# Kernel tuning notes

Hardware: AMD Instinct MI355X
Metric: run time of the kernel (lower is better)

Reference implementation:

```python
import jax, jax.numpy as jnp
import numpy as np
from jax import lax

# ---- static config (matches init_kwargs) ----
STRIDE = 16
BASE_SIZE = 16
SCALES = np.array([2., 4., 8., 16., 32.])
RATIOS = np.array([0.5, 1., 2.])
CLIP = 4.14
NMS_THRESH = 0.7
PRE_NMS = 6000
POST_NMS = 300
MIN_SIZE = 16.0


def _whctrs(a):
    w = a[2] - a[0] + 1.0
    h = a[3] - a[1] + 1.0
    return w, h, a[0] + 0.5 * (w - 1.0), a[1] + 0.5 * (h - 1.0)


def _mkanchors(ws, hs, xc, yc):
    return np.stack([xc - 0.5 * (ws - 1.0), yc - 0.5 * (hs - 1.0),
                     xc + 0.5 * (ws - 1.0), yc + 0.5 * (hs - 1.0)], axis=1)


def _base_anchors():
    ba = np.array([1.0, 1.0, BASE_SIZE, BASE_SIZE]) - 1.0
    w, h, xc, yc = _whctrs(ba)
    size = w * h
    ws = np.round(np.sqrt(size / RATIOS))
    hs = np.round(ws * RATIOS)
    ra = _mkanchors(ws, hs, xc, yc)
    out = []
    for i in range(ra.shape[0]):
        w, h, xc, yc = _whctrs(ra[i])
        out.append(_mkanchors(w * SCALES, h * SCALES, xc, yc))
    return np.concatenate(out, axis=0)  # (A,4), A = len(ratios)*len(scales)


def _grid_anchors(Hf, Wf):
    ba = _base_anchors()                       # (A,4)
    sx, sy = np.meshgrid(np.arange(Wf) * STRIDE, np.arange(Hf) * STRIDE)
    shifts = np.stack([sx, sy, sx, sy], axis=-1)          # (Hf,Wf,4)
    anch = shifts[:, :, None, :] + ba[None, None, :, :]    # (Hf,Wf,A,4)
    return jnp.asarray(anch.reshape(1, -1, 4), dtype=jnp.float32)


def _decode_clip(anchors, deltas, img_h, img_w):
    # NormalizedBoxCenterDecoder (stds=1) + clip to image
    aw = anchors[..., 2] - anchors[..., 0]
    ah = anchors[..., 3] - anchors[..., 1]
    ax = anchors[..., 0] + 0.5 * aw
    ay = anchors[..., 1] + 0.5 * ah
    dx, dy, dw, dh = deltas[..., 0], deltas[..., 1], deltas[..., 2], deltas[..., 3]
    ox = dx * aw + ax
    oy = dy * ah + ay
    ow = jnp.exp(jnp.minimum(dw, CLIP)) * aw * 0.5
    oh = jnp.exp(jnp.minimum(dh, CLIP)) * ah * 0.5
    x1 = jnp.clip(ox - ow, 0.0, img_w - 1.0)
    y1 = jnp.clip(oy - oh, 0.0, img_h - 1.0)
    x2 = jnp.clip(ox + ow, 0.0, img_w - 1.0)
    y2 = jnp.clip(oy + oh, 0.0, img_h - 1.0)
    return jnp.stack([x1, y1, x2, y2], axis=-1)


def _nms_single(scores, boxes):
    # scores (N,), boxes (N,4). Greedy NMS, force_suppress, sorted by score desc.
    order = jnp.argsort(-scores)[:PRE_NMS]
    s = scores[order]
    b = boxes[order]
    x1, y1, x2, y2 = b[:, 0], b[:, 1], b[:, 2], b[:, 3]
    area = (x2 - x1) * (y2 - y1)
    iw = jnp.maximum(jnp.minimum(x2[:, None], x2[None, :]) - jnp.maximum(x1[:, None], x1[None, :]), 0.0)
    ih = jnp.maximum(jnp.minimum(y2[:, None], y2[None, :]) - jnp.maximum(y1[:, None], y1[None, :]), 0.0)
    inter = iw * ih
    iou = inter / (area[:, None] + area[None, :] - inter + 1e-12)  # (PRE,PRE)

    supp0 = s < 0.0  # invalid entries (score set to -1 by min_size filter)

    def body(supp, i):
        keep = jnp.logical_not(supp[i])
        new = jnp.where(keep, jnp.logical_or(supp, iou[i] > NMS_THRESH), supp)
        new = new.at[i].set(supp[i])  # never self-suppress
        return new, None

    supp, _ = lax.scan(body, supp0, jnp.arange(PRE_NMS))
    kept = jnp.logical_not(supp)
    perm = jnp.argsort(jnp.where(kept, 0, 1), stable=True)  # kept boxes first, order preserved
    out_s = jnp.where(kept[perm], s[perm], -1.0)
    out_b = jnp.where(kept[perm][:, None], b[perm], -1.0)
    return out_s[:POST_NMS, None], out_b[:POST_NMS]


def _forward(img, x, conv_w, conv_b, score_w, score_b, loc_w, loc_b):
    B, _, Hf, Wf = x.shape
    img_h, img_w = float(img.shape[2]), float(img.shape[3])
    anchors = _grid_anchors(Hf, Wf)  # (1, Hf*Wf*A, 4)

    # conv1 3x3 pad 1 + ReLU
    h = lax.conv_general_dilated(x, conv_w, (1, 1), [(1, 1), (1, 1)],
                                 dimension_numbers=('NCHW', 'OIHW', 'NCHW'))
    h = jax.nn.relu(h + conv_b[None, :, None, None])

    A = score_w.shape[0]
    raw_scores = jnp.einsum('bchw,oc->bhwo', h, score_w.reshape(A, -1)) + score_b
    raw_scores = raw_scores.reshape(B, -1, 1)                       # (B,N,1)
    raw_boxes = jnp.einsum('bchw,oc->bhwo', h, loc_w.reshape(4 * A, -1)) + loc_b
    raw_boxes = raw_boxes.reshape(B, -1, 4)                         # (B,N,4)

    rpn_scores = jax.nn.sigmoid(raw_scores)

    roi = _decode_clip(anchors, raw_boxes, img_h, img_w)            # (B,N,4)
    width = roi[..., 2] - roi[..., 0]
    height = roi[..., 3] - roi[..., 1]
    invalid = jnp.logical_or(width < MIN_SIZE, height < MIN_SIZE)   # (B,N)
    score = jnp.where(invalid[..., None], -1.0, rpn_scores)         # (B,N,1)
    roi = jnp.where(invalid[..., None], -1.0, roi)

    out_s, out_b = jax.vmap(_nms_single)(score[..., 0], roi)        # (B,300,1),(B,300,4)
    return jnp.concatenate([out_s, out_b], axis=-1)                 # (B,300,5)


def setup_inputs() -> dict:
    key = jax.random.key(0)
    ks = jax.random.split(key, 8)
    img = jax.random.normal(ks[0], (1, 3, 1024, 1024), jnp.float32)
    x = jax.random.normal(ks[1], (1, 1024, 64, 64), jnp.float32)
    conv_w = jax.random.normal(ks[2], (1024, 1024, 3, 3), jnp.float32) * 0.01
    conv_b = jnp.zeros((1024,), jnp.float32)
    score_w = jax.random.normal(ks[3], (15, 1024, 1, 1), jnp.float32) * 0.01
    score_b = jnp.zeros((15,), jnp.float32)
    loc_w = jax.random.normal(ks[4], (60, 1024, 1, 1), jnp.float32) * 0.002
    loc_b = jnp.zeros((60,), jnp.float32)
    return {"img": img, "x": x, "conv_w": conv_w, "conv_b": conv_b,
            "score_w": score_w, "score_b": score_b, "loc_w": loc_w, "loc_b": loc_b}


def reference(img, x, conv_w, conv_b, score_w, score_b, loc_w, loc_b):
    return _forward(img, x, conv_w, conv_b, score_w, score_b, loc_w, loc_b)
```

## Files before the change

### kernel.cpp

```cpp
#include <hip/hip_runtime.h>

typedef unsigned int uint;
typedef unsigned short ushort;
typedef unsigned long long u64;

typedef __attribute__((ext_vector_type(8))) short short8;
typedef __attribute__((ext_vector_type(4))) float floatx4;

__device__ inline ushort bf16rne(float v) {
  uint b = __float_as_uint(v);
  uint r = (b + 0x7fffu + ((b >> 16) & 1u)) >> 16;
  return (ushort)r;
}

__device__ inline void gl_lds16(const void* g, void* l) {
  __builtin_amdgcn_global_load_lds(
      (const __attribute__((address_space(1))) unsigned int*)g,
      (__attribute__((address_space(3))) unsigned int*)l, 16, 0, 0);
}


__global__ __launch_bounds__(256) void prep_x(const float* __restrict__ x,
                                              ushort* __restrict__ xh,
                                              ushort* __restrict__ xl) {
  __shared__ float tile[8][512];
  int cc = blockIdx.x, sg = blockIdx.y, t = threadIdx.x;
  int ci0 = cc * 32 + sg * 8;
  size_t obase = (size_t)(cc * 4 + sg) * 4356;
  for (int it = 0; it < 4; ++it) {
    int s0 = blockIdx.z * 2048 + it * 512;
#pragma unroll
    for (int e = 0; e < 8; ++e) {
      tile[e][t] = x[(size_t)(ci0 + e) * 4096 + s0 + t];
      tile[e][t + 256] = x[(size_t)(ci0 + e) * 4096 + s0 + 256 + t];
    }
    __syncthreads();
#pragma unroll
    for (int w = 0; w < 2; ++w) {
      int sl = w * 256 + t;
      int s = s0 + sl;
      int y = s >> 6, xx = s & 63;
      short8 sh, slo;
#pragma unroll
      for (int e = 0; e < 8; ++e) {
        float v = tile[e][sl];
        ushort h2 = bf16rne(v);
        float hf = __uint_as_float((uint)h2 << 16);
        sh[e] = (short)h2;
        slo[e] = (short)bf16rne(v - hf);
      }
      size_t o = (obase + (size_t)(y + 1) * 66 + (xx + 1)) * 8;
      *(short8*)(xh + o) = sh;
      *(short8*)(xl + o) = slo;
    }
    __syncthreads();
  }
}

__global__ __launch_bounds__(256) void prep_w(const float* __restrict__ w,
                                              ushort* __restrict__ wh,
                                              ushort* __restrict__ wl) {
  int cc = blockIdx.x, sg = blockIdx.y, t = threadIdx.x;
  int e = t & 7, col = t >> 3;
  int ci = cc * 32 + sg * 8 + e;
  for (int chunk = 0; chunk < 8; ++chunk) {
    int co = blockIdx.z * 256 + chunk * 32 + col;
    const float* src = w + ((size_t)co * 1024 + ci) * 9;
    float v[9];
#pragma unroll
    for (int o = 0; o < 9; ++o) v[o] = src[o];
#pragma unroll
    for (int off = 0; off < 9; ++off) {
      ushort h2 = bf16rne(v[off]);
      float hf = __uint_as_float((uint)h2 << 16);
      ushort l2 = bf16rne(v[off] - hf);
      size_t oi = ((size_t)(off * 32 + cc) * 4 + sg) * 8192 + (size_t)co * 8 + e;
      wh[oi] = h2;
      wl[oi] = l2;
    }
  }
}

__global__ __launch_bounds__(256) void prep_head(
    const float* __restrict__ score_w, const float* __restrict__ loc_w,
    const float* __restrict__ score_b, const float* __restrict__ loc_b,
    ushort* __restrict__ wh, ushort* __restrict__ wl, float* __restrict__ bh) {
  int idx = blockIdx.x * 256 + threadIdx.x;
  int o = idx >> 10, ci = idx & 1023;
  float v = 0.f;
  if (o < 15) v = score_w[o * 1024 + ci];
  else if (o < 75) v = loc_w[(o - 15) * 1024 + ci];
  ushort h2 = bf16rne(v);
  float hf = __uint_as_float((uint)h2 << 16);
  int cc = ci >> 5, sg = (ci >> 3) & 3, e = ci & 7;
  size_t oi = ((size_t)(cc * 4 + sg) * 128 + o) * 8 + e;
  wh[oi] = h2;
  wl[oi] = bf16rne(v - hf);
  if (idx < 128) bh[idx] = (idx < 15) ? score_b[idx] : ((idx < 75) ? loc_b[idx - 15] : 0.f);
}

template <int IM2COL, int BM, int BN>
__global__ __launch_bounds__(256, 1) void gemm_bf16x3(
    const ushort* __restrict__ Ahi, const ushort* __restrict__ Alo,
    const ushort* __restrict__ Bhi, const ushort* __restrict__ Blo,
    const float* __restrict__ bias, int nChunks, float* __restrict__ outRaw,
    ushort* __restrict__ outHi, ushort* __restrict__ outLo) {
  constexpr int ASEC = BM * 32;
  constexpr int BUFU = 2 * ASEC;
  constexpr int WM = (BM >= 128) ? 2 : 1;
  constexpr int WN = 4 / WM;
  constexpr int MI = (BM / WM) / 16;
  constexpr int NJ = (BN / WN) / 16;
  __shared__ ushort sm[2 * BUFU];
  const int t = threadIdx.x;
  const int m0 = blockIdx.x * BM;
  const int n0 = blockIdx.y * BN;

  const int lane = t & 63, wv = t >> 6;
  const int wm = (wv % WM) * (BM / WM);
  const int wn = (wv / WM) * (BN / WN);
  const int rA = wm + (lane & 15);
  const int segA = (lane >> 4) * (BM * 16);

  auto stage = [&](int c, int bufIdx) {
    ushort* secAh = sm + bufIdx * BUFU;
    ushort* secAl = secAh + ASEC;
    int cc = 0, oy = 0, ox = 0;
    if (IM2COL) {
      int off = c >> 5;
      cc = c & 31;
      oy = off / 3;
      ox = off - 3 * oy;
    }
    for (int L = t; L < BM * 4; L += 256) {
      int row = L % BM, seg = L / BM;
      size_t aoff;
      if (IM2COL) {
        int m = m0 + row, y = m >> 6, xq = m & 63;
        aoff = ((size_t)(cc * 4 + seg) * 4356 + (y + oy) * 66 + (xq + ox)) * 16;
      } else {
        aoff = ((size_t)(c * 4 + seg) * 4096 + (m0 + row)) * 16;
      }
      gl_lds16((const char*)Ahi + aoff, (char*)secAh + L * 16);
      gl_lds16((const char*)Alo + aoff, (char*)secAl + L * 16);
    }
  };

  auto loadB = [&](int c, short8* bh, short8* bl) {
    int sg = lane >> 4;
#pragma unroll
    for (int j = 0; j < NJ; ++j) {
      int co = n0 + wn + (lane & 15) + 16 * j;
      size_t boff;
      if (IM2COL) {
        int off = c >> 5, cc = c & 31;
        boff = (((size_t)(off * 32 + cc) * 4 + sg) * 1024 + co) * 16;
      } else {
        boff = (((size_t)(c * 4 + sg)) * 128 + co) * 16;
      }
      bh[j] = *(const short8*)((const char*)Bhi + boff);
      bl[j] = *(const short8*)((const char*)Blo + boff);
    }
  };

  floatx4 acc[MI][NJ];
#pragma unroll
  for (int i = 0; i < MI; ++i)
#pragma unroll
    for (int j = 0; j < NJ; ++j) acc[i][j] = (floatx4){0.f, 0.f, 0.f, 0.f};

  auto compute = [&](const ushort* sb, const short8* bh2, const short8* bl2) {
    const char* cAh = (const char*)sb;
    const char* cAl = (const char*)(sb + ASEC);
    short8 ah[MI], al[MI];
#pragma unroll
    for (int i = 0; i < MI; ++i) {
      int pa = segA + (rA + 16 * i) * 16;
      ah[i] = *(const short8*)(cAh + pa);
      al[i] = *(const short8*)(cAl + pa);
    }
#pragma unroll
    for (int i = 0; i < MI; ++i)
#pragma unroll
      for (int j = 0; j < NJ; ++j) {
        acc[i][j] = __builtin_amdgcn_mfma_f32_16x16x32_bf16(ah[i], bh2[j], acc[i][j], 0, 0, 0);
        acc[i][j] = __builtin_amdgcn_mfma_f32_16x16x32_bf16(ah[i], bl2[j], acc[i][j], 0, 0, 0);
        acc[i][j] = __builtin_amdgcn_mfma_f32_16x16x32_bf16(al[i], bh2[j], acc[i][j], 0, 0, 0);
      }
  };

  short8 b0h[NJ], b0l[NJ], b1h[NJ], b1l[NJ];
  stage(0, 0);
  loadB(0, b0h, b0l);
  for (int kc = 0; kc < nChunks; kc += 2) {
    __syncthreads();
    if (kc + 1 < nChunks) { stage(kc + 1, 1); loadB(kc + 1, b1h, b1l); }
    compute(sm, b0h, b0l);
    __syncthreads();
    if (kc + 2 < nChunks) { stage(kc + 2, 0); loadB(kc + 2, b0h, b0l); }
    compute(sm + BUFU, b1h, b1l);
  }

#pragma unroll
  for (int i = 0; i < MI; ++i)
#pragma unroll
    for (int j = 0; j < NJ; ++j) {
      int nn = n0 + wn + 16 * j + (lane & 15);
      float bv = bias[nn];
#pragma unroll
      for (int r = 0; r < 4; ++r) {
        int mm = m0 + wm + 16 * i + (lane >> 4) * 4 + r;
        float v = acc[i][j][r] + bv;
        if (IM2COL) {
          v = fmaxf(v, 0.f);
          ushort h2 = bf16rne(v);
          float hf = __uint_as_float((uint)h2 << 16);
          ushort l2 = bf16rne(v - hf);
          int cc = nn >> 5, sg = (nn >> 3) & 3, e = nn & 7;
          size_t ho = ((size_t)(cc * 4 + sg) * 4096 + mm) * 8 + e;
          outHi[ho] = h2;
          outLo[ho] = l2;
        } else {
          outRaw[(size_t)mm * 128 + nn] = v;
        }
      }
    }
}

__global__ __launch_bounds__(256) void decode_k(const float* __restrict__ raw,
                                                float* __restrict__ scores,
                                                float4* __restrict__ boxes,
                                                uint* __restrict__ key32,
                                                uint* __restrict__ hist) {
  int i = blockIdx.x * 256 + threadIdx.x;
  int m = i / 15, a = i - m * 15;
  int y = m >> 6, x = m & 63;
  const float* rp = raw + (size_t)m * 128;
  float logit = rp[a];
  float dx = rp[15 + 4 * a], dy = rp[16 + 4 * a];
  float dw = rp[17 + 4 * a], dh = rp[18 + 4 * a];
  int rr = a / 5, ss = a - rr * 5;
  float sc5 = (float)(2 << ss);
  float W = ((rr == 0) ? 23.f : (rr == 1) ? 16.f : 11.f) * sc5;
  float H = ((rr == 0) ? 12.f : (rr == 1) ? 16.f : 22.f) * sc5;
  float aw = W - 1.f, ah = H - 1.f;
  float ax = x * 16.f + 7.5f, ay = y * 16.f + 7.5f;
  float ox = dx * aw + ax, oyc = dy * ah + ay;
  float ow = expf(fminf(dw, 4.14f)) * aw * 0.5f;
  float oh = expf(fminf(dh, 4.14f)) * ah * 0.5f;
  float x1 = fminf(fmaxf(ox - ow, 0.f), 1023.f);
  float y1 = fminf(fmaxf(oyc - oh, 0.f), 1023.f);
  float x2 = fminf(fmaxf(ox + ow, 0.f), 1023.f);
  float y2 = fminf(fmaxf(oyc + oh, 0.f), 1023.f);
  bool inval = ((x2 - x1) < 16.f) || ((y2 - y1) < 16.f);
  float sc = inval ? -1.f : (1.f / (1.f + expf(-logit)));
  scores[i] = sc;
  boxes[i] = inval ? make_float4(-1.f, -1.f, -1.f, -1.f) : make_float4(x1, y1, x2, y2);
  uint kb = __float_as_uint(sc);
  uint key = (kb & 0x80000000u) ? ~kb : (kb | 0x80000000u);
  key32[i] = key;
  atomicAdd(&hist[key >> 16], 1u);
}

__global__ __launch_bounds__(256) void seg_sum(const uint* __restrict__ hist,
                                               uint* __restrict__ segsum) {
  __shared__ uint red[256];
  int b = blockIdx.x, t = threadIdx.x;
  red[t] = hist[b * 256 + t];
  __syncthreads();
  for (int d = 128; d > 0; d >>= 1) {
    if (t < d) red[t] += red[t + d];
    __syncthreads();
  }
  if (t == 0) segsum[b] = red[0];
}

__global__ __launch_bounds__(256) void find_t16(const uint* __restrict__ hist,
                                                const uint* __restrict__ segsum,
                                                uint* __restrict__ selT) {
  __shared__ uint ps[256];
  __shared__ int segS;
  int t = threadIdx.x;
  ps[t] = segsum[t];
  __syncthreads();
  for (int d = 1; d < 256; d <<= 1) {
    uint v = ps[t] + ((t + d < 256) ? ps[t + d] : 0u);
    __syncthreads();
    ps[t] = v;
    __syncthreads();
  }
  if (ps[t] >= 6000u && (t == 255 || ps[t + 1] < 6000u)) segS = t;
  __syncthreads();
  int sg = segS;
  uint base = (sg == 255) ? 0u : ps[sg + 1];
  uint h2 = hist[sg * 256 + t];
  __syncthreads();
  ps[t] = h2;
  __syncthreads();
  for (int d = 1; d < 256; d <<= 1) {
    uint v = ps[t] + ((t + d < 256) ? ps[t + d] : 0u);
    __syncthreads();
    ps[t] = v;
    __syncthreads();
  }
  if (base + ps[t] >= 6000u && (t == 255 || base + ps[t + 1] < 6000u))
    *selT = (uint)(sg * 256 + t);
}

__global__ __launch_bounds__(256) void gather_k(const uint* __restrict__ key32,
                                                const uint* __restrict__ selT,
                                                uint* __restrict__ cnt,
                                                u64* __restrict__ cand) {
  int i = blockIdx.x * 256 + threadIdx.x;
  uint T = *selT;
  uint k = key32[i];
  if ((k >> 16) >= T) {
    uint pos = atomicAdd(cnt, 1u);
    if (pos < 8192) cand[pos] = ((u64)k << 32) | (u64)(~(uint)i);
  }
}

__global__ __launch_bounds__(1024) void sort_gather(
    const u64* __restrict__ cand, const uint* __restrict__ cnt,
    const float* __restrict__ scores, const float4* __restrict__ boxes,
    float* __restrict__ sortedS, float4* __restrict__ sortedB) {
  extern __shared__ u64 sk[];
  int t = threadIdx.x;
  int C = (int)*cnt;
  if (C > 8192) C = 8192;
  for (int j = t; j < 8192; j += 1024) sk[j] = (j < C) ? cand[j] : 0ull;
  __syncthreads();
  for (int k = 2; k <= 8192; k <<= 1) {
    for (int j2 = k >> 1; j2 > 0; j2 >>= 1) {
      for (int p = t; p < 4096; p += 1024) {
        int i = ((p & ~(j2 - 1)) << 1) | (p & (j2 - 1));
        int ix = i | j2;
        u64 a = sk[i], b = sk[ix];
        bool ddir = (i & k) != 0;
        if ((a < b) != ddir) { sk[i] = b; sk[ix] = a; }
      }
      __syncthreads();
    }
  }
  for (int j = t; j < 6016; j += 1024) {
    if (j < 6000) {
      u64 key = sk[j];
      uint idx = ~(uint)(key & 0xffffffffu);
      sortedS[j] = scores[idx];
      sortedB[j] = boxes[idx];
    } else {
      sortedS[j] = -1.f;
      sortedB[j] = make_float4(0.f, 0.f, 0.f, 0.f);
    }
  }
}

__global__ __launch_bounds__(64) void iou_mask(const float4* __restrict__ boxes,
                                               u64* __restrict__ mask) {
  __shared__ float cx1[64], cy1[64], cx2[64], cy2[64], car[64];
  int bi = blockIdx.x, bj = blockIdx.y, t = threadIdx.x;
  float4 cb = boxes[bj * 64 + t];
  cx1[t] = cb.x; cy1[t] = cb.y; cx2[t] = cb.z; cy2[t] = cb.w;
  car[t] = (cb.z - cb.x) * (cb.w - cb.y);
  __syncthreads();
  int r = bi * 64 + t;
  float4 rb = boxes[r];
  float ra = (rb.z - rb.x) * (rb.w - rb.y);
  u64 wd = 0;
#pragma unroll 8
  for (int j = 0; j < 64; ++j) {
    float iw = fmaxf(fminf(rb.z, cx2[j]) - fmaxf(rb.x, cx1[j]), 0.f);
    float ih = fmaxf(fminf(rb.w, cy2[j]) - fmaxf(rb.y, cy1[j]), 0.f);
    float inter = iw * ih;
    float iou = inter / (ra + car[j] - inter + 1e-12f);
    if (iou > 0.7f && r != bj * 64 + j) wd |= (1ull << j);
  }
  mask[(size_t)r * 128 + bj] = wd;
}

__global__ __launch_bounds__(64) void nms_scan(const u64* __restrict__ mask,
                                               const float* __restrict__ sortedS,
                                               const float4* __restrict__ sortedB,
                                               float* __restrict__ out) {
  __shared__ int klist[300];
  int lane = threadIdx.x;
  u64 Sx = 0, Sy = 0;
  for (int w2 = 0; w2 < 94; ++w2) {
    bool neg = sortedS[w2 * 64 + lane] < 0.f;
    u64 m2 = __ballot(neg);
    if ((w2 >> 1) == lane) { if (w2 & 1) Sy = m2; else Sx = m2; }
  }
  int count = 0;
  for (int w2 = 0; w2 < 94; ++w2) {
    u64 cur = __shfl((w2 & 1) ? Sy : Sx, w2 >> 1);
    u64 rem = ~cur;
    if (w2 == 93) rem &= (1ull << 48) - 1;
    if (!rem) continue;
    int bA = __builtin_ctzll(rem);
    ulonglong2 vA = ((const ulonglong2*)(mask + (size_t)(w2 * 64 + bA) * 128))[lane];
    int bB;
    ulonglong2 vB;
    for (;;) {
      {
        u64 remS = (bA == 63) ? 0ull : (rem & (~0ull << (bA + 1)));
        bB = remS ? __builtin_ctzll(remS) : -1;
        if (bB >= 0)
          vB = ((const ulonglong2*)(mask + (size_t)(w2 * 64 + bB) * 128))[lane];
        if (lane == 0) klist[count] = w2 * 64 + bA;
        count++;
        if (count == 300) goto done;
        Sx |= vA.x;
        Sy |= vA.y;
        u64 cur2 = __shfl((w2 & 1) ? Sy : Sx, w2 >> 1);
        rem = remS & ~cur2;
        if (!rem) break;
        int bn = __builtin_ctzll(rem);
        if (bn != bB) {
          bB = bn;
          vB = ((const ulonglong2*)(mask + (size_t)(w2 * 64 + bB) * 128))[lane];
        }
      }
      {
        u64 remS = (bB == 63) ? 0ull : (rem & (~0ull << (bB + 1)));
        bA = remS ? __builtin_ctzll(remS) : -1;
        if (bA >= 0)
          vA = ((const ulonglong2*)(mask + (size_t)(w2 * 64 + bA) * 128))[lane];
        if (lane == 0) klist[count] = w2 * 64 + bB;
        count++;
        if (count == 300) goto done;
        Sx |= vB.x;
        Sy |= vB.y;
        u64 cur2 = __shfl((w2 & 1) ? Sy : Sx, w2 >> 1);
        rem = remS & ~cur2;
        if (!rem) break;
        int bn = __builtin_ctzll(rem);
        if (bn != bA) {
          bA = bn;
          vA = ((const ulonglong2*)(mask + (size_t)(w2 * 64 + bA) * 128))[lane];
        }
      }
    }
  }
done:
  __syncthreads();
  for (int j = lane; j < 300; j += 64) {
    float s;
    float4 bb;
    if (j < count) {
      int i = klist[j];
      s = sortedS[i];
      bb = sortedB[i];
    } else {
      s = -1.f;
      bb = make_float4(-1.f, -1.f, -1.f, -1.f);
    }
    out[j * 5 + 0] = s;
    out[j * 5 + 1] = bb.x;
    out[j * 5 + 2] = bb.y;
    out[j * 5 + 3] = bb.z;
    out[j * 5 + 4] = bb.w;
  }
}

constexpr size_t O_XH = 0;
constexpr size_t O_XL = 8921088;
constexpr size_t O_WTH = 17842176;
constexpr size_t O_WTL = 36716544;
constexpr size_t O_HH = 55590912;
constexpr size_t O_HL = 63979520;
constexpr size_t O_WHH = 72368128;
constexpr size_t O_WHL = 72630272;
constexpr size_t O_BHD = 72892416;
constexpr size_t O_SC = 72892928;
constexpr size_t O_BX = 73138688;
constexpr size_t O_KEY = 74121728;
constexpr size_t O_HIST = 74367488;
constexpr size_t O_CNT = 74629632;
constexpr size_t O_CAND = 74629888;
constexpr size_t O_SELT = 74695424;
constexpr size_t O_SS = 74695680;
constexpr size_t O_SB = 74719744;
constexpr size_t O_RAW = 0;
constexpr size_t O_MASK = 17842176;
constexpr size_t O_SEG = 24002560;

extern "C" void kernel_launch(void* const* d_in, const int* in_sizes, int n_in,
                              void* d_out, int out_size, void* d_ws,
                              size_t ws_size, hipStream_t stream) {
  (void)in_sizes; (void)n_in; (void)out_size; (void)ws_size;
  const float* x = (const float*)d_in[1];
  const float* conv_w = (const float*)d_in[2];
  const float* conv_b = (const float*)d_in[3];
  const float* score_w = (const float*)d_in[4];
  const float* score_b = (const float*)d_in[5];
  const float* loc_w = (const float*)d_in[6];
  const float* loc_b = (const float*)d_in[7];
  float* out = (float*)d_out;
  char* ws = (char*)d_ws;

  ushort* xh = (ushort*)(ws + O_XH);
  ushort* xl = (ushort*)(ws + O_XL);
  ushort* wTh = (ushort*)(ws + O_WTH);
  ushort* wTl = (ushort*)(ws + O_WTL);
  ushort* hh = (ushort*)(ws + O_HH);
  ushort* hl = (ushort*)(ws + O_HL);
  ushort* wHh = (ushort*)(ws + O_WHH);
  ushort* wHl = (ushort*)(ws + O_WHL);
  float* biasH = (float*)(ws + O_BHD);
  float* raw = (float*)(ws + O_RAW);
  float* scores = (float*)(ws + O_SC);
  float4* boxes = (float4*)(ws + O_BX);
  uint* key32 = (uint*)(ws + O_KEY);
  uint* hist = (uint*)(ws + O_HIST);
  uint* cnt = (uint*)(ws + O_CNT);
  u64* cand = (u64*)(ws + O_CAND);
  uint* selT = (uint*)(ws + O_SELT);
  float* sortedS = (float*)(ws + O_SS);
  float4* sortedB = (float4*)(ws + O_SB);
  u64* mask = (u64*)(ws + O_MASK);
  uint* segsum = (uint*)(ws + O_SEG);

  hipMemsetAsync(ws + O_XH, 0, 2 * 8921088, stream);
  hipMemsetAsync(ws + O_HIST, 0, 262144 + 256, stream);

  prep_x<<<dim3(32, 4, 2), 256, 0, stream>>>(x, xh, xl);
  prep_w<<<dim3(32, 4, 4), 256, 0, stream>>>(conv_w, wTh, wTl);
  prep_head<<<512, 256, 0, stream>>>(score_w, loc_w, score_b, loc_b, wHh, wHl, biasH);

  gemm_bf16x3<1, 128, 64><<<dim3(32, 16), 256, 0, stream>>>(
      xh, xl, wTh, wTl, conv_b, 288, nullptr, hh, hl);
  gemm_bf16x3<0, 32, 128><<<dim3(128, 1), 256, 0, stream>>>(
      hh, hl, wHh, wHl, biasH, 32, raw, nullptr, nullptr);

  decode_k<<<240, 256, 0, stream>>>(raw, scores, boxes, key32, hist);
  seg_sum<<<256, 256, 0, stream>>>(hist, segsum);
  find_t16<<<1, 256, 0, stream>>>(hist, segsum, selT);
  gather_k<<<240, 256, 0, stream>>>(key32, selT, cnt, cand);
  sort_gather<<<1, 1024, 65536, stream>>>(cand, cnt, scores, boxes, sortedS, sortedB);
  iou_mask<<<dim3(94, 94), 64, 0, stream>>>(sortedB, mask);
  nms_scan<<<1, 64, 0, stream>>>(mask, sortedS, sortedB, out);
}
```

Baseline: 715.3 us.

## Split conv GEMM into triple-buffered kernel staging B through LDS

The 3x3 conv GEMM gets its own kernel. Both A and B tiles now stream into LDS through async global-to-LDS loads, with a three-deep ring buffer and explicit vmcnt waits, so there is one barrier per K chunk instead of register-loaded B with double buffering. Launch bounds now allow two blocks per CU. The head GEMM keeps the old path. The aim is to hide global memory latency and raise occupancy, at the cost of more LDS use per block and fragile hand-tuned waitcnt ordering.

```diff
diff --git a/kernel.cpp b/kernel.cpp
--- a/kernel.cpp
+++ b/kernel.cpp
@@ -99,12 +99,132 @@
   if (idx < 128) bh[idx] = (idx < 15) ? score_b[idx] : ((idx < 75) ? loc_b[idx - 15] : 0.f);
 }
 
-template <int IM2COL, int BM, int BN>
-__global__ __launch_bounds__(256, 1) void gemm_bf16x3(
+__global__ __launch_bounds__(256, 2) void gemm_conv(
     const ushort* __restrict__ Ahi, const ushort* __restrict__ Alo,
     const ushort* __restrict__ Bhi, const ushort* __restrict__ Blo,
-    const float* __restrict__ bias, int nChunks, float* __restrict__ outRaw,
-    ushort* __restrict__ outHi, ushort* __restrict__ outLo) {
+    const float* __restrict__ bias, ushort* __restrict__ outHi,
+    ushort* __restrict__ outLo) {
+  constexpr int NC = 288;
+  constexpr int ASEC = 128 * 32;
+  constexpr int BSEC = 64 * 32;
+  constexpr int BUFU = 2 * ASEC + 2 * BSEC;
+  __shared__ ushort sm[3 * BUFU];
+  const int t = threadIdx.x;
+  const int m0 = blockIdx.x * 128;
+  const int n0 = blockIdx.y * 64;
+
+  const int lane = t & 63, wv = t >> 6;
+  const int wm = (wv & 1) * 64, wn = (wv >> 1) * 32;
+  const int rA = wm + (lane & 15);
+  const int rB = wn + (lane & 15);
+  const int segA = (lane >> 4) * 2048;
+  const int segB = (lane >> 4) * 1024;
+
+  auto stage = [&](int c, ushort* buf) {
+    ushort* secAh = buf;
+    ushort* secAl = buf + ASEC;
+    ushort* secBh = buf + 2 * ASEC;
+    ushort* secBl = buf + 2 * ASEC + BSEC;
+    int off = c >> 5, cc = c & 31;
+    int oy = off / 3, ox = off - 3 * oy;
+#pragma unroll
+    for (int q = 0; q < 2; ++q) {
+      int L = t + 256 * q;
+      int row = L & 127, seg = L >> 7;
+      int m = m0 + row, y = m >> 6, xq = m & 63;
+      size_t aoff = ((size_t)(cc * 4 + seg) * 4356 + (y + oy) * 66 + (xq + ox)) * 16;
+      gl_lds16((const char*)Ahi + aoff, (char*)secAh + L * 16);
+      gl_lds16((const char*)Alo + aoff, (char*)secAl + L * 16);
+    }
+    {
+      int L = t;
+      int row = L & 63, seg = L >> 6;
+      size_t boff = (((size_t)(off * 32 + cc) * 4 + seg) * 1024 + (n0 + row)) * 16;
+      gl_lds16((const char*)Bhi + boff, (char*)secBh + L * 16);
+      gl_lds16((const char*)Blo + boff, (char*)secBl + L * 16);
+    }
+  };
+
+  floatx4 acc[4][2];
+#pragma unroll
+  for (int i = 0; i < 4; ++i)
+#pragma unroll
+    for (int j = 0; j < 2; ++j) acc[i][j] = (floatx4){0.f, 0.f, 0.f, 0.f};
+
+  auto compute = [&](const ushort* sb) {
+    const char* cAh = (const char*)sb;
+    const char* cAl = (const char*)(sb + ASEC);
+    const char* cBh = (const char*)(sb + 2 * ASEC);
+    const char* cBl = (const char*)(sb + 2 * ASEC + BSEC);
+    short8 ah[4], al[4], bh2[2], bl2[2];
+#pragma unroll
+    for (int i = 0; i < 4; ++i) {
+      int pa = segA + (rA + 16 * i) * 16;
+      ah[i] = *(const short8*)(cAh + pa);
+      al[i] = *(const short8*)(cAl + pa);
+    }
+#pragma unroll
+    for (int j = 0; j < 2; ++j) {
+      int pb = segB + (rB + 16 * j) * 16;
+      bh2[j] = *(const short8*)(cBh + pb);
+      bl2[j] = *(const short8*)(cBl + pb);
+    }
+#pragma unroll
+    for (int i = 0; i < 4; ++i)
+#pragma unroll
+      for (int j = 0; j < 2; ++j) {
+        acc[i][j] = __builtin_amdgcn_mfma_f32_16x16x32_bf16(ah[i], bh2[j], acc[i][j], 0, 0, 0);
+        acc[i][j] = __builtin_amdgcn_mfma_f32_16x16x32_bf16(ah[i], bl2[j], acc[i][j], 0, 0, 0);
+        acc[i][j] = __builtin_amdgcn_mfma_f32_16x16x32_bf16(al[i], bh2[j], acc[i][j], 0, 0, 0);
+      }
+  };
+
+  stage(0, sm);
+  stage(1, sm + BUFU);
+  int br = 0;
+  int bw = 2;
+  for (int kc = 0; kc < NC; ++kc) {
+    __builtin_amdgcn_sched_barrier(0);
+    if (kc < NC - 1) {
+      asm volatile("s_waitcnt vmcnt(6)" ::: "memory");
+    } else {
+      asm volatile("s_waitcnt vmcnt(0)" ::: "memory");
+    }
+    __builtin_amdgcn_sched_barrier(0);
+    __builtin_amdgcn_s_barrier();
+    __builtin_amdgcn_sched_barrier(0);
+    if (kc + 2 < NC) stage(kc + 2, sm + bw * BUFU);
+    compute(sm + br * BUFU);
+    br = (br == 2) ? 0 : br + 1;
+    bw = (bw == 2) ? 0 : bw + 1;
+  }
+
+#pragma unroll
+  for (int i = 0; i < 4; ++i)
+#pragma unroll
+    for (int j = 0; j < 2; ++j) {
+      int nn = n0 + wn + 16 * j + (lane & 15);
+      float bv = bias[nn];
+#pragma unroll
+      for (int r = 0; r < 4; ++r) {
+        int mm = m0 + wm + 16 * i + (lane >> 4) * 4 + r;
+        float v = fmaxf(acc[i][j][r] + bv, 0.f);
+        ushort h2 = bf16rne(v);
+        float hf = __uint_as_float((uint)h2 << 16);
+        ushort l2 = bf16rne(v - hf);
+        int cc = nn >> 5, sg = (nn >> 3) & 3, e = nn & 7;
+        size_t ho = ((size_t)(cc * 4 + sg) * 4096 + mm) * 8 + e;
+        outHi[ho] = h2;
+        outLo[ho] = l2;
+      }
+    }
+}
+
+template <int BM, int BN>
+__global__ __launch_bounds__(256, 1) void gemm_head(
+    const ushort* __restrict__ Ahi, const ushort* __restrict__ Alo,
+    const ushort* __restrict__ Bhi, const ushort* __restrict__ Blo,
+    const float* __restrict__ bias, int nChunks, float* __restrict__ outRaw) {
   constexpr int ASEC = BM * 32;
   constexpr int BUFU = 2 * ASEC;
   constexpr int WM = (BM >= 128) ? 2 : 1;
@@ -125,22 +245,9 @@
   auto stage = [&](int c, int bufIdx) {
     ushort* secAh = sm + bufIdx * BUFU;
     ushort* secAl = secAh + ASEC;
-    int cc = 0, oy = 0, ox = 0;
-    if (IM2COL) {
-      int off = c >> 5;
-      cc = c & 31;
-      oy = off / 3;
-      ox = off - 3 * oy;
-    }
     for (int L = t; L < BM * 4; L += 256) {
       int row = L % BM, seg = L / BM;
-      size_t aoff;
-      if (IM2COL) {
-        int m = m0 + row, y = m >> 6, xq = m & 63;
-        aoff = ((size_t)(cc * 4 + seg) * 4356 + (y + oy) * 66 + (xq + ox)) * 16;
-      } else {
-        aoff = ((size_t)(c * 4 + seg) * 4096 + (m0 + row)) * 16;
-      }
+      size_t aoff = ((size_t)(c * 4 + seg) * 4096 + (m0 + row)) * 16;
       gl_lds16((const char*)Ahi + aoff, (char*)secAh + L * 16);
       gl_lds16((const char*)Alo + aoff, (char*)secAl + L * 16);
     }
@@ -151,13 +258,7 @@
 #pragma unroll
     for (int j = 0; j < NJ; ++j) {
       int co = n0 + wn + (lane & 15) + 16 * j;
-      size_t boff;
-      if (IM2COL) {
-        int off = c >> 5, cc = c & 31;
-        boff = (((size_t)(off * 32 + cc) * 4 + sg) * 1024 + co) * 16;
-      } else {
-        boff = (((size_t)(c * 4 + sg)) * 128 + co) * 16;
-      }
+      size_t boff = (((size_t)(c * 4 + sg)) * 128 + co) * 16;
       bh[j] = *(const short8*)((const char*)Bhi + boff);
       bl[j] = *(const short8*)((const char*)Blo + boff);
     }
@@ -210,19 +311,7 @@
 #pragma unroll
       for (int r = 0; r < 4; ++r) {
         int mm = m0 + wm + 16 * i + (lane >> 4) * 4 + r;
-        float v = acc[i][j][r] + bv;
-        if (IM2COL) {
-          v = fmaxf(v, 0.f);
-          ushort h2 = bf16rne(v);
-          float hf = __uint_as_float((uint)h2 << 16);
-          ushort l2 = bf16rne(v - hf);
-          int cc = nn >> 5, sg = (nn >> 3) & 3, e = nn & 7;
-          size_t ho = ((size_t)(cc * 4 + sg) * 4096 + mm) * 8 + e;
-          outHi[ho] = h2;
-          outLo[ho] = l2;
-        } else {
-          outRaw[(size_t)mm * 128 + nn] = v;
-        }
+        outRaw[(size_t)mm * 128 + nn] = acc[i][j][r] + bv;
       }
     }
 }
@@ -527,10 +616,9 @@
   prep_w<<<dim3(32, 4, 4), 256, 0, stream>>>(conv_w, wTh, wTl);
   prep_head<<<512, 256, 0, stream>>>(score_w, loc_w, score_b, loc_b, wHh, wHl, biasH);
 
-  gemm_bf16x3<1, 128, 64><<<dim3(32, 16), 256, 0, stream>>>(
-      xh, xl, wTh, wTl, conv_b, 288, nullptr, hh, hl);
-  gemm_bf16x3<0, 32, 128><<<dim3(128, 1), 256, 0, stream>>>(
-      hh, hl, wHh, wHl, biasH, 32, raw, nullptr, nullptr);
+  gemm_conv<<<dim3(32, 16), 256, 0, stream>>>(xh, xl, wTh, wTl, conv_b, hh, hl);
+  gemm_head<32, 128><<<dim3(128, 1), 256, 0, stream>>>(hh, hl, wHh, wHl, biasH,
+                                                       32, raw);
 
   decode_k<<<240, 256, 0, stream>>>(raw, scores, boxes, key32, hist);
   seg_sum<<<256, 256, 0, stream>>>(hist, segsum);
```

New measurement: 705.5 us. No clear change (-1.4%).
